# Performance work log

Measured on AMD Instinct MI355X. Metric: run time of the kernel, lower is better.

The kernel has to match this reference:

```python
import jax, jax.numpy as jnp
import numpy as np

PRUNE_N = 2
PRUNE_M = 4


def _semi_structural_prune(x_flat):
    """Keep the PRUNE_N largest-|.| elements in every contiguous group of PRUNE_M."""
    n_tok, d = x_flat.shape
    x1d = x_flat.reshape(-1, PRUNE_M)                      # [G, 4]
    _, idx = jax.lax.top_k(jnp.abs(x1d), PRUNE_N)          # [G, 2]
    rows = jnp.arange(x1d.shape[0])[:, None]
    mask = jnp.zeros_like(x1d).at[rows, idx].set(1.0)      # scatter ones -> 2:4 mask
    return (x1d * mask).reshape(n_tok, d)


def setup_inputs() -> dict:
    key = jax.random.key(0)
    k1, k2 = jax.random.split(key)
    x = jax.random.normal(k1, (4, 4096, 2048), dtype=jnp.float32)
    weight = jax.random.normal(k2, (2048, 2048), dtype=jnp.float32) * 0.02
    return {"x": x, "weight": weight}


def reference(x, weight):
    bs, seq_len, d = x.shape
    x_flat = x.reshape(-1, d)                              # [bs*seq, d]
    x_sp = _semi_structural_prune(x_flat)
    # variance correction: v = sqrt(var(x) / clamp(var(x_sp), 1e-9)); torch.var -> ddof=1
    var_ratio = jnp.var(x_flat, ddof=1) / jnp.maximum(jnp.var(x_sp, ddof=1), 1e-9)
    v = jnp.sqrt(var_ratio)
    out = (v * x_sp) @ weight.T                            # [bs*seq, out_features]
    return out.reshape(bs, seq_len, -1)
```

## Files before the change

kernel.cpp:

```cpp
#include <hip/hip_runtime.h>
#include <stdint.h>

typedef unsigned short u16;
typedef __attribute__((ext_vector_type(4))) unsigned short u16x4;
typedef __attribute__((ext_vector_type(4))) float f32x4;
typedef __attribute__((ext_vector_type(8))) __bf16 bf16x8;

#define M_DIM 16384
#define N_DIM 2048
#define K_DIM 2048
#define NELEM (M_DIM * K_DIM)
#define NGROUPS (NELEM / 4)
#define WELEM (N_DIM * K_DIM)
#define PRUNE_BLOCKS 2048
#define PRUNE_ITERS (NGROUPS / (PRUNE_BLOCKS * 256))

__device__ __forceinline__ u16 f2bf(float f) {
    union { float f; uint32_t u; } c; c.f = f;
    uint32_t r = c.u + 0x7FFFu + ((c.u >> 16) & 1u);
    return (u16)(r >> 16);
}

__global__ __launch_bounds__(256) void prune_kernel(const float* __restrict__ x,
                                                    u16* __restrict__ xsp,
                                                    float4* __restrict__ partials) {
    float sx = 0.f, sxx = 0.f, sp = 0.f, spp = 0.f;
    int g = blockIdx.x * 256 + threadIdx.x;
    const int stride = PRUNE_BLOCKS * 256;
#pragma unroll 4
    for (int it = 0; it < PRUNE_ITERS; ++it, g += stride) {
        float4 v = ((const float4*)x)[g];
        float a0 = v.x, a1 = v.y, a2 = v.z, a3 = v.w;
        float b0 = fabsf(a0), b1 = fabsf(a1), b2 = fabsf(a2), b3 = fabsf(a3);
        int r0 = (b1 > b0) + (b2 > b0) + (b3 > b0);
        int r1 = (b0 >= b1) + (b2 > b1) + (b3 > b1);
        int r2 = (b0 >= b2) + (b1 >= b2) + (b3 > b2);
        int r3 = (b0 >= b3) + (b1 >= b3) + (b2 >= b3);
        float k0 = (r0 < 2) ? a0 : 0.f;
        float k1 = (r1 < 2) ? a1 : 0.f;
        float k2 = (r2 < 2) ? a2 : 0.f;
        float k3 = (r3 < 2) ? a3 : 0.f;
        sx  += a0 + a1 + a2 + a3;
        sxx += a0*a0 + a1*a1 + a2*a2 + a3*a3;
        sp  += k0 + k1 + k2 + k3;
        spp += k0*k0 + k1*k1 + k2*k2 + k3*k3;
        u16x4 o;
        o.x = f2bf(k0); o.y = f2bf(k1); o.z = f2bf(k2); o.w = f2bf(k3);
        ((u16x4*)xsp)[g] = o;
    }
    for (int off = 32; off > 0; off >>= 1) {
        sx  += __shfl_down(sx,  off, 64);
        sxx += __shfl_down(sxx, off, 64);
        sp  += __shfl_down(sp,  off, 64);
        spp += __shfl_down(spp, off, 64);
    }
    __shared__ float red[4][4];
    int wid = threadIdx.x >> 6, lane = threadIdx.x & 63;
    if (lane == 0) { red[wid][0] = sx; red[wid][1] = sxx; red[wid][2] = sp; red[wid][3] = spp; }
    __syncthreads();
    if (threadIdx.x == 0) {
        float4 t;
        t.x = red[0][0] + red[1][0] + red[2][0] + red[3][0];
        t.y = red[0][1] + red[1][1] + red[2][1] + red[3][1];
        t.z = red[0][2] + red[1][2] + red[2][2] + red[3][2];
        t.w = red[0][3] + red[1][3] + red[2][3] + red[3][3];
        partials[blockIdx.x] = t;
    }
}

__global__ __launch_bounds__(256) void finalize_kernel(const float4* __restrict__ partials,
                                                       float* __restrict__ vout) {
    float sx = 0.f, sxx = 0.f, sp = 0.f, spp = 0.f;
#pragma unroll
    for (int i = 0; i < PRUNE_BLOCKS / 256; ++i) {
        float4 t = partials[i * 256 + threadIdx.x];
        sx += t.x; sxx += t.y; sp += t.z; spp += t.w;
    }
    for (int off = 32; off > 0; off >>= 1) {
        sx  += __shfl_down(sx,  off, 64);
        sxx += __shfl_down(sxx, off, 64);
        sp  += __shfl_down(sp,  off, 64);
        spp += __shfl_down(spp, off, 64);
    }
    __shared__ float red[4][4];
    int wid = threadIdx.x >> 6, lane = threadIdx.x & 63;
    if (lane == 0) { red[wid][0] = sx; red[wid][1] = sxx; red[wid][2] = sp; red[wid][3] = spp; }
    __syncthreads();
    if (threadIdx.x == 0) {
        float tsx  = red[0][0] + red[1][0] + red[2][0] + red[3][0];
        float tsxx = red[0][1] + red[1][1] + red[2][1] + red[3][1];
        float tsp  = red[0][2] + red[1][2] + red[2][2] + red[3][2];
        float tspp = red[0][3] + red[1][3] + red[2][3] + red[3][3];
        const float n = (float)NELEM;
        float varx = (tsxx - tsx * tsx / n) / (n - 1.f);
        float varp = (tspp - tsp * tsp / n) / (n - 1.f);
        varp = fmaxf(varp, 1e-9f);
        vout[0] = sqrtf(varx / varp);
    }
}

__global__ __launch_bounds__(256) void wconv_kernel(const float* __restrict__ w,
                                                    u16* __restrict__ wb) {
    int i = blockIdx.x * 256 + threadIdx.x;
    float4 v = ((const float4*)w)[i];
    u16x4 o;
    o.x = f2bf(v.x); o.y = f2bf(v.y); o.z = f2bf(v.z); o.w = f2bf(v.w);
    ((u16x4*)wb)[i] = o;
}

#define GLD16(g, l) \
    __builtin_amdgcn_global_load_lds((__attribute__((address_space(1))) void*)(g), \
                                     (__attribute__((address_space(3))) void*)(l), 16, 0, 0)

__global__ __launch_bounds__(256) void gemm_kernel(const u16* __restrict__ A,
                                                   const u16* __restrict__ B,
                                                   const float* __restrict__ vscale,
                                                   float* __restrict__ out) {
    __shared__ __align__(16) u16 As[128 * 32];
    __shared__ __align__(16) u16 Bs[128 * 32];

    const int tid  = threadIdx.x;
    const int lane = tid & 63;
    const int wid  = tid >> 6;
    const int wm   = (wid >> 1) * 64;
    const int wn   = (wid & 1) * 64;
    const int l15  = lane & 15;
    const int quad = lane >> 4;

    const int b    = blockIdx.x;
    const int xcd  = b & 7;
    const int s    = b >> 3;
    const int mrow = xcd * 16 + (s >> 4);
    const int ncol = s & 15;
    const int m0 = mrow * 128;
    const int n0 = ncol * 128;

    const int idx0 = tid;
    const int idx1 = tid + 256;
    const int rA0 = idx0 >> 2, sA0 = (idx0 & 3) * 8;
    const int rA1 = idx1 >> 2, sA1 = (idx1 & 3) * 8;
    const u16* gA0 = A + (size_t)(m0 + rA0) * K_DIM + sA0;
    const u16* gA1 = A + (size_t)(m0 + rA1) * K_DIM + sA1;
    const u16* gB0 = B + (size_t)(n0 + rA0) * K_DIM + sA0;
    const u16* gB1 = B + (size_t)(n0 + rA1) * K_DIM + sA1;

    f32x4 acc[4][4] = {};

    for (int kt = 0; kt < K_DIM / 32; ++kt) {
        GLD16(gA0, &As[idx0 * 8]);
        GLD16(gA1, &As[idx1 * 8]);
        GLD16(gB0, &Bs[idx0 * 8]);
        GLD16(gB1, &Bs[idx1 * 8]);
        gA0 += 32; gA1 += 32; gB0 += 32; gB1 += 32;
        __syncthreads();

        const bf16x8* Ap = (const bf16x8*)As;
        const bf16x8* Bp = (const bf16x8*)Bs;
        bf16x8 aF[4], bF[4];
#pragma unroll
        for (int i = 0; i < 4; ++i)
            aF[i] = Ap[(wm + i * 16 + l15) * 4 + quad];
#pragma unroll
        for (int j = 0; j < 4; ++j)
            bF[j] = Bp[(wn + j * 16 + l15) * 4 + quad];
#pragma unroll
        for (int i = 0; i < 4; ++i)
#pragma unroll
            for (int j = 0; j < 4; ++j)
                acc[i][j] = __builtin_amdgcn_mfma_f32_16x16x32_bf16(aF[i], bF[j], acc[i][j], 0, 0, 0);
        __syncthreads();
    }

    const float v = vscale[0];

    float* op = out + (size_t)(m0 + wm) * N_DIM + n0 + wn;
#pragma unroll
    for (int i = 0; i < 4; ++i)
#pragma unroll
        for (int j = 0; j < 4; ++j)
#pragma unroll
            for (int r = 0; r < 4; ++r)
                op[(size_t)(i * 16 + quad * 4 + r) * N_DIM + j * 16 + l15] = acc[i][j][r] * v;
}

extern "C" void kernel_launch(void* const* d_in, const int* in_sizes, int n_in,
                              void* d_out, int out_size, void* d_ws, size_t ws_size,
                              hipStream_t stream) {
    const float* x = (const float*)d_in[0];
    const float* w = (const float*)d_in[1];
    float* out = (float*)d_out;

    u16* xsp      = (u16*)d_ws;
    u16* wb       = xsp + NELEM;
    float4* parts = (float4*)(wb + WELEM);
    float* vbuf   = (float*)(parts + PRUNE_BLOCKS);

    prune_kernel<<<PRUNE_BLOCKS, 256, 0, stream>>>(x, xsp, parts);
    finalize_kernel<<<1, 256, 0, stream>>>(parts, vbuf);
    wconv_kernel<<<WELEM / 4 / 256, 256, 0, stream>>>(w, wb);
    gemm_kernel<<<2048, 256, 0, stream>>>(xsp, wb, vbuf, out);
}
```

Baseline: 392.6 us.

## Rewrite GEMM as 256x256 tile, 8-wave, double-buffered swizzled-LDS pipeline

```diff
diff --git a/kernel.cpp b/kernel.cpp
--- a/kernel.cpp
+++ b/kernel.cpp
@@ -112,70 +112,155 @@
     __builtin_amdgcn_global_load_lds((__attribute__((address_space(1))) void*)(g), \
                                      (__attribute__((address_space(3))) void*)(l), 16, 0, 0)
 
-__global__ __launch_bounds__(256) void gemm_kernel(const u16* __restrict__ A,
-                                                   const u16* __restrict__ B,
-                                                   const float* __restrict__ vscale,
-                                                   float* __restrict__ out) {
-    __shared__ __align__(16) u16 As[128 * 32];
-    __shared__ __align__(16) u16 Bs[128 * 32];
+#define STG(gb, ldsA, bufq, hf, kt) do { \
+    const u16* _g = (gb) + (size_t)(hf) * (128 * K_DIM) + (size_t)(kt) * 64; \
+    u16* _l = &(ldsA)[bufq][(hf) * 128][0] + ldst; \
+    GLD16(_g, _l); \
+    GLD16(_g + 64 * K_DIM, _l + 64 * 64); \
+} while (0)
+
+#define MM(va, vb, c) (c) = __builtin_amdgcn_mfma_f32_16x16x32_bf16((va), (vb), (c), 0, 0, 0)
+
+__global__ __launch_bounds__(512, 2) void gemm_kernel(const u16* __restrict__ A,
+                                                      const u16* __restrict__ B,
+                                                      const float* __restrict__ vscale,
+                                                      float* __restrict__ out) {
+    __shared__ __align__(16) u16 As[2][256][64];
+    __shared__ __align__(16) u16 Bs[2][256][64];
 
     const int tid  = threadIdx.x;
     const int lane = tid & 63;
-    const int wid  = tid >> 6;
-    const int wm   = (wid >> 1) * 64;
-    const int wn   = (wid & 1) * 64;
     const int l15  = lane & 15;
     const int quad = lane >> 4;
+    const int wid  = tid >> 6;
+    const int wm   = wid >> 2;
+    const int wn   = (wid & 3) * 64;
 
     const int b    = blockIdx.x;
     const int xcd  = b & 7;
     const int s    = b >> 3;
-    const int mrow = xcd * 16 + (s >> 4);
-    const int ncol = s & 15;
-    const int m0 = mrow * 128;
-    const int n0 = ncol * 128;
-
-    const int idx0 = tid;
-    const int idx1 = tid + 256;
-    const int rA0 = idx0 >> 2, sA0 = (idx0 & 3) * 8;
-    const int rA1 = idx1 >> 2, sA1 = (idx1 & 3) * 8;
-    const u16* gA0 = A + (size_t)(m0 + rA0) * K_DIM + sA0;
-    const u16* gA1 = A + (size_t)(m0 + rA1) * K_DIM + sA1;
-    const u16* gB0 = B + (size_t)(n0 + rA0) * K_DIM + sA0;
-    const u16* gB1 = B + (size_t)(n0 + rA1) * K_DIM + sA1;
-
-    f32x4 acc[4][4] = {};
-
-    for (int kt = 0; kt < K_DIM / 32; ++kt) {
-        GLD16(gA0, &As[idx0 * 8]);
-        GLD16(gA1, &As[idx1 * 8]);
-        GLD16(gB0, &Bs[idx0 * 8]);
-        GLD16(gB1, &Bs[idx1 * 8]);
-        gA0 += 32; gA1 += 32; gB0 += 32; gB1 += 32;
-        __syncthreads();
-
-        const bf16x8* Ap = (const bf16x8*)As;
-        const bf16x8* Bp = (const bf16x8*)Bs;
-        bf16x8 aF[4], bF[4];
-#pragma unroll
-        for (int i = 0; i < 4; ++i)
-            aF[i] = Ap[(wm + i * 16 + l15) * 4 + quad];
-#pragma unroll
-        for (int j = 0; j < 4; ++j)
-            bF[j] = Bp[(wn + j * 16 + l15) * 4 + quad];
-#pragma unroll
-        for (int i = 0; i < 4; ++i)
-#pragma unroll
-            for (int j = 0; j < 4; ++j)
-                acc[i][j] = __builtin_amdgcn_mfma_f32_16x16x32_bf16(aF[i], bF[j], acc[i][j], 0, 0, 0);
-        __syncthreads();
-    }
+    const int m0   = (xcd * 8 + (s >> 3)) * 256;
+    const int n0   = (s & 7) * 256;
+
+    const int r0   = tid >> 3;
+    const int slot = tid & 7;
+    const int srcs = slot ^ (r0 & 7);
+    const int ldst = tid * 8;
+    const u16* Ab = A + (size_t)(m0 + r0) * K_DIM + srcs * 8;
+    const u16* Bb = B + (size_t)(n0 + r0) * K_DIM + srcs * 8;
+
+    const int rsw  = (l15 & 7) << 4;
+    const int xk0  = (quad * 16) ^ rsw;
+    const int xk1  = (64 + quad * 16) ^ rsw;
+    const int aRow = (wm * 128 + l15) * 128;
+    const int bRow = (wn + l15) * 128;
 
     const float v = vscale[0];
 
-    float* op = out + (size_t)(m0 + wm) * N_DIM + n0 + wn;
-#pragma unroll
-    for (int i = 0; i < 4; ++i)
+    f32x4 acc[8][4] = {};
+    bf16x8 aF[4][2], bF[2][2], bG[2][2];
+
+    STG(Ab, As, 0, 0, 0);
+    STG(Ab, As, 0, 1, 0);
+    STG(Bb, Bs, 0, 0, 0);
+    STG(Bb, Bs, 0, 1, 0);
+    STG(Ab, As, 1, 0, 1);
+    asm volatile("s_waitcnt vmcnt(2)" ::: "memory");
+    __builtin_amdgcn_sched_barrier(0);
+    __builtin_amdgcn_s_barrier();
+
+    const int NKT = K_DIM / 64;
+    for (int t = 0; t < NKT; ++t) {
+        const int pb  = (t & 1) * 32768;
+        const char* pA = (const char*)As + pb + aRow;
+        const char* pB = (const char*)Bs + pb + bRow;
+        const int nb  = (t + 1) & 1;
+
+#pragma unroll
+        for (int i = 0; i < 4; ++i) {
+            aF[i][0] = *(const bf16x8*)(pA + i * 2048 + xk0);
+            aF[i][1] = *(const bf16x8*)(pA + i * 2048 + xk1);
+        }
+#pragma unroll
+        for (int j = 0; j < 2; ++j) {
+            bF[j][0] = *(const bf16x8*)(pB + j * 2048 + xk0);
+            bF[j][1] = *(const bf16x8*)(pB + j * 2048 + xk1);
+        }
+        if (t + 1 < NKT) STG(Ab, As, nb, 1, t + 1);
+        __builtin_amdgcn_s_barrier();
+        asm volatile("s_waitcnt lgkmcnt(0)" ::: "memory");
+        __builtin_amdgcn_sched_barrier(0);
+        __builtin_amdgcn_s_setprio(1);
+#pragma unroll
+        for (int i = 0; i < 4; ++i)
+#pragma unroll
+            for (int j = 0; j < 2; ++j) {
+                MM(aF[i][0], bF[j][0], acc[i][j]);
+                MM(aF[i][1], bF[j][1], acc[i][j]);
+            }
+        __builtin_amdgcn_s_setprio(0);
+        __builtin_amdgcn_s_barrier();
+
+#pragma unroll
+        for (int j = 0; j < 2; ++j) {
+            bG[j][0] = *(const bf16x8*)(pB + 4096 + j * 2048 + xk0);
+            bG[j][1] = *(const bf16x8*)(pB + 4096 + j * 2048 + xk1);
+        }
+        if (t + 1 < NKT) STG(Bb, Bs, nb, 0, t + 1);
+        __builtin_amdgcn_s_barrier();
+        asm volatile("s_waitcnt lgkmcnt(0)" ::: "memory");
+        __builtin_amdgcn_sched_barrier(0);
+        __builtin_amdgcn_s_setprio(1);
+#pragma unroll
+        for (int i = 0; i < 4; ++i)
+#pragma unroll
+            for (int j = 0; j < 2; ++j) {
+                MM(aF[i][0], bG[j][0], acc[i][2 + j]);
+                MM(aF[i][1], bG[j][1], acc[i][2 + j]);
+            }
+        __builtin_amdgcn_s_setprio(0);
+        __builtin_amdgcn_s_barrier();
+
+#pragma unroll
+        for (int i = 0; i < 4; ++i) {
+            aF[i][0] = *(const bf16x8*)(pA + 8192 + i * 2048 + xk0);
+            aF[i][1] = *(const bf16x8*)(pA + 8192 + i * 2048 + xk1);
+        }
+        if (t + 1 < NKT) STG(Bb, Bs, nb, 1, t + 1);
+        __builtin_amdgcn_s_barrier();
+        asm volatile("s_waitcnt lgkmcnt(0)" ::: "memory");
+        __builtin_amdgcn_sched_barrier(0);
+        __builtin_amdgcn_s_setprio(1);
+#pragma unroll
+        for (int i = 0; i < 4; ++i)
+#pragma unroll
+            for (int j = 0; j < 2; ++j) {
+                MM(aF[i][0], bF[j][0], acc[4 + i][j]);
+                MM(aF[i][1], bF[j][1], acc[4 + i][j]);
+            }
+        __builtin_amdgcn_s_setprio(0);
+        __builtin_amdgcn_s_barrier();
+
+        if (t + 2 < NKT) STG(Ab, As, t & 1, 0, t + 2);
+        __builtin_amdgcn_s_barrier();
+        __builtin_amdgcn_s_setprio(1);
+#pragma unroll
+        for (int i = 0; i < 4; ++i)
+#pragma unroll
+            for (int j = 0; j < 2; ++j) {
+                MM(aF[i][0], bG[j][0], acc[4 + i][2 + j]);
+                MM(aF[i][1], bG[j][1], acc[4 + i][2 + j]);
+            }
+        __builtin_amdgcn_s_setprio(0);
+        if (t + 2 < NKT) { asm volatile("s_waitcnt vmcnt(2)" ::: "memory"); }
+        else             { asm volatile("s_waitcnt vmcnt(0)" ::: "memory"); }
+        __builtin_amdgcn_sched_barrier(0);
+        __builtin_amdgcn_s_barrier();
+    }
+
+    float* op = out + (size_t)(m0 + wm * 128) * N_DIM + n0 + wn;
+#pragma unroll
+    for (int i = 0; i < 8; ++i)
 #pragma unroll
         for (int j = 0; j < 4; ++j)
 #pragma unroll
@@ -198,5 +283,5 @@
     prune_kernel<<<PRUNE_BLOCKS, 256, 0, stream>>>(x, xsp, parts);
     finalize_kernel<<<1, 256, 0, stream>>>(parts, vbuf);
     wconv_kernel<<<WELEM / 4 / 256, 256, 0, stream>>>(w, wb);
-    gemm_kernel<<<2048, 256, 0, stream>>>(xsp, wb, vbuf, out);
-}
+    gemm_kernel<<<512, 512, 0, stream>>>(xsp, wb, vbuf, out);
+}
```

New measurement: 378.7 us. 1.04x faster.
